# Kernel optimization log

Measured on AMD Instinct MI355X. Metric: run time of the kernel, lower is better.

## Reference

```python
import jax, jax.numpy as jnp
import numpy as np

T, B, D_POSE, H, K_CODES = 30, 1024, 135, 512, 512
EPS = 1e-5


def _bn_relu(x, g, b):
    # BatchNorm1d (training-mode batch stats, biased var) + ReLU; x: (B, C, L)
    m = x.mean(axis=(0, 2), keepdims=True)
    v = x.var(axis=(0, 2), keepdims=True)
    y = g[None, :, None] * (x - m) * jax.lax.rsqrt(v + EPS) + b[None, :, None]
    return jax.nn.relu(y)


def _conv_sk(x, w):
    # Conv1d with stride == kernel_size (non-overlapping): pure reshaped GEMM.
    # x: (B, I, L), w: (O, I, K) torch layout -> (B, O, L//K)
    Bn, I, L = x.shape
    O, _, K = w.shape
    xr = x.reshape(Bn, I, L // K, K)
    return jnp.einsum('bitk,oik->bot', xr, w)


def _convT_sk(x, w):
    # ConvTranspose1d with stride == kernel_size: x (B, I, L), w (I, O, K) torch layout
    Bn, I, L = x.shape
    _, O, K = w.shape
    return jnp.einsum('bil,iok->bolk', x, w).reshape(Bn, O, L * K)


def setup_inputs() -> dict:
    key = jax.random.key(0)
    ks = jax.random.split(key, 12)
    sc = 0.05
    inp = {
        'input_seqs': jax.random.normal(ks[0], (T, B, D_POSE), jnp.float32),
        'W_in': jax.random.normal(ks[1], (D_POSE, H), jnp.float32) * sc,
        'b_in': jnp.zeros((H,), jnp.float32),
        'w_e1': jax.random.normal(ks[2], (H, H, 5), jnp.float32) * sc,
        'g_e1': jnp.ones((H,), jnp.float32), 'b_e1': jnp.zeros((H,), jnp.float32),
        'w_e2': jax.random.normal(ks[3], (H, H, 3), jnp.float32) * sc,
        'g_e2': jnp.ones((H,), jnp.float32), 'b_e2': jnp.zeros((H,), jnp.float32),
        'w_e3': jax.random.normal(ks[4], (H, H, 2), jnp.float32) * sc,
        'g_e3': jnp.ones((H,), jnp.float32), 'b_e3': jnp.zeros((H,), jnp.float32),
        'codebook': jax.random.normal(ks[5], (K_CODES, H), jnp.float32) * sc,
        'W_q': jax.random.normal(ks[6], (H, H), jnp.float32) * sc,
        'b_q': jnp.zeros((H,), jnp.float32),
        'w_d1': jax.random.normal(ks[7], (H, H, 2), jnp.float32) * sc,
        'g_d1': jnp.ones((H,), jnp.float32), 'b_d1': jnp.zeros((H,), jnp.float32),
        'w_d2': jax.random.normal(ks[8], (H, H, 3), jnp.float32) * sc,
        'g_d2': jnp.ones((H,), jnp.float32), 'b_d2': jnp.zeros((H,), jnp.float32),
        'w_d3': jax.random.normal(ks[9], (H, H, 5), jnp.float32) * sc,
        'g_d3': jnp.ones((H,), jnp.float32), 'b_d3': jnp.zeros((H,), jnp.float32),
        'W_out': jax.random.normal(ks[10], (H, D_POSE), jnp.float32) * sc,
        'b_out': jnp.zeros((D_POSE,), jnp.float32),
    }
    return inp


def reference(input_seqs, W_in, b_in, w_e1, g_e1, b_e1, w_e2, g_e2, b_e2,
              w_e3, g_e3, b_e3, codebook, W_q, b_q,
              w_d1, g_d1, b_d1, w_d2, g_d2, b_d2, w_d3, g_d3, b_d3,
              W_out, b_out):
    commitment_cost = 0.25
    # ---- EncoderCNN ----
    h = input_seqs @ W_in + b_in              # (T, B, H)
    h = jnp.transpose(h, (1, 2, 0))           # (B, H, T)
    h = _bn_relu(_conv_sk(h, w_e1), g_e1, b_e1)   # (B, H, 6)
    h = _bn_relu(_conv_sk(h, w_e2), g_e2, b_e2)   # (B, H, 2)
    z = _bn_relu(_conv_sk(h, w_e3), g_e3, b_e3)   # (B, H, 1)

    # ---- VQ (VQ_Payam, straight-through) ----
    Bn, D, L = z.shape
    flat = jnp.transpose(z, (0, 2, 1)).reshape(-1, D)            # (B*L, D)
    dist = (jnp.sum(flat ** 2, axis=1, keepdims=True)
            + jnp.sum(codebook ** 2, axis=1)
            - 2.0 * flat @ codebook.T)                           # (B*L, K)
    idx = jnp.argmin(dist, axis=1)                               # (B*L,)
    quantized = codebook[idx]                                    # (B*L, D)
    e_latent_loss = jnp.mean((jax.lax.stop_gradient(quantized) - flat) ** 2)
    q_latent_loss = jnp.mean((quantized - jax.lax.stop_gradient(flat)) ** 2)
    vq_loss = q_latent_loss + commitment_cost * e_latent_loss
    q_st = flat + jax.lax.stop_gradient(quantized - flat)        # straight-through
    avg_probs = jnp.mean(jax.nn.one_hot(idx, K_CODES, dtype=flat.dtype), axis=0)
    perplexity = jnp.exp(-jnp.sum(avg_probs * jnp.log(avg_probs + 1e-10)))

    # ---- DecoderCNN ----
    d = q_st @ W_q + b_q                      # (B, H)
    d = d[:, :, None]                         # (B, H, 1)
    d = _bn_relu(_convT_sk(d, w_d1), g_d1, b_d1)  # (B, H, 2)
    d = _bn_relu(_convT_sk(d, w_d2), g_d2, b_d2)  # (B, H, 6)
    d = _bn_relu(_convT_sk(d, w_d3), g_d3, b_d3)  # (B, H, 30)
    recon = jnp.transpose(d, (0, 2, 1)) @ W_out + b_out           # (B, T, D_POSE)
    return recon, vq_loss, perplexity
```

## Files before the change

kernel.cpp:

```cpp
#include <hip/hip_runtime.h>
#include <math.h>


typedef __attribute__((ext_vector_type(8))) short bf16x8;
typedef __attribute__((ext_vector_type(4))) float f32x4;

__device__ __forceinline__ unsigned pk_bf16(float a, float b) {
    unsigned ua = __float_as_uint(a), ub = __float_as_uint(b);
    ua += 0x7fffu + ((ua >> 16) & 1u);
    ub += 0x7fffu + ((ub >> 16) & 1u);
    return (ua >> 16) | (ub & 0xffff0000u);
}
__device__ __forceinline__ unsigned short bfh(float x) {
    unsigned u = __float_as_uint(x);
    u += 0x7fffu + ((u >> 16) & 1u);
    return (unsigned short)(u >> 16);
}
__device__ __forceinline__ float bf2f(unsigned short h) {
    return __uint_as_float(((unsigned)h) << 16);
}

template <int NV>
__device__ __forceinline__ void bn_on_raw(uint4* raw, int kbase,
                                          const float* __restrict__ bnS,
                                          const float* __restrict__ bnB) {
#pragma unroll
    for (int i = 0; i < NV; ++i) {
        unsigned* u4 = (unsigned*)&raw[i];
#pragma unroll
        for (int j = 0; j < 4; ++j) {
            const int k = kbase + (i << 3) + (j << 1);
            unsigned u = u4[j];
            float x0 = __uint_as_float(u << 16);
            float x1 = __uint_as_float(u & 0xffff0000u);
            x0 = fmaxf(fmaf(x0, bnS[k],     bnB[k]),     0.f);
            x1 = fmaxf(fmaf(x1, bnS[k + 1], bnB[k + 1]), 0.f);
            u4[j] = pk_bf16(x0, x1);
        }
    }
}

__device__ __forceinline__ void bn4(float4& a, const float* __restrict__ s,
                                    const float* __restrict__ c) {
    float4 sv = *(const float4*)s;
    float4 cv = *(const float4*)c;
    a.x = fmaxf(fmaf(a.x, sv.x, cv.x), 0.f);
    a.y = fmaxf(fmaf(a.y, sv.y, cv.y), 0.f);
    a.z = fmaxf(fmaf(a.z, sv.z, cv.z), 0.f);
    a.w = fmaxf(fmaf(a.w, sv.w, cv.w), 0.f);
}

#define FBK  32
#define FSTR 36

__global__ __launch_bounds__(256)
void k_gemm(const float* __restrict__ Abase,
            const float* __restrict__ Wt,
            float* __restrict__ Cout,
            const float* __restrict__ bnS, const float* __restrict__ bnB,
            unsigned long long* __restrict__ amin,
            const float* __restrict__ codesq,
            int Mslice, int K, int N, int decK)
{
    __shared__ __align__(16) float As[FBK][FSTR];
    __shared__ __align__(16) float Bs[FBK][FSTR];

    const int tid = threadIdx.x;
    const int z  = blockIdx.z;
    const int n0 = blockIdx.x << 5;
    const int m0 = blockIdx.y << 5;
    const int ty = tid >> 4;
    const int tx = tid & 15;

    const int a_slice = z / decK, wk = z - a_slice * decK;
    const float* Ap = Abase + (size_t)a_slice * (size_t)Mslice * (size_t)K;
    const float* Wp = Wt    + (size_t)wk * (size_t)K * (size_t)N;

    const int sr  = tid >> 3;
    const int sc4 = (tid & 7) << 2;

    int mrow = m0 + sr;
    if (mrow > Mslice - 1) mrow = Mslice - 1;
    const float* Arow_p = Ap + (size_t)mrow * K;

    float acc[2][2];
    acc[0][0] = 0.f; acc[0][1] = 0.f; acc[1][0] = 0.f; acc[1][1] = 0.f;

    float4 pa = *(const float4*)(Arow_p + sc4);
    if (bnS != nullptr) bn4(pa, bnS + sc4, bnB + sc4);
    float4 pb = *(const float4*)(Wp + (size_t)sr * N + n0 + sc4);

    for (int k0 = 0; k0 < K; k0 += FBK) {
        __syncthreads();
        As[sc4 + 0][sr] = pa.x;
        As[sc4 + 1][sr] = pa.y;
        As[sc4 + 2][sr] = pa.z;
        As[sc4 + 3][sr] = pa.w;
        *(float4*)&Bs[sr][sc4] = pb;
        const int k0n = k0 + FBK;
        if (k0n < K) {
            pa = *(const float4*)(Arow_p + k0n + sc4);
            if (bnS != nullptr) bn4(pa, bnS + k0n + sc4, bnB + k0n + sc4);
            pb = *(const float4*)(Wp + (size_t)(k0n + sr) * N + n0 + sc4);
        }
        __syncthreads();
#pragma unroll
        for (int kk = 0; kk < FBK; ++kk) {
            float2 av = *(const float2*)&As[kk][ty << 1];
            float2 bv = *(const float2*)&Bs[kk][tx << 1];
            acc[0][0] = fmaf(av.x, bv.x, acc[0][0]);
            acc[0][1] = fmaf(av.x, bv.y, acc[0][1]);
            acc[1][0] = fmaf(av.y, bv.x, acc[1][0]);
            acc[1][1] = fmaf(av.y, bv.y, acc[1][1]);
        }
    }

    if (amin != nullptr) {
        float2 cq = *(const float2*)(codesq + n0 + (tx << 1));
#pragma unroll
        for (int i = 0; i < 2; ++i) {
            const int m = m0 + (ty << 1) + i;
            float d0 = cq.x - 2.f * acc[i][0];
            float d1 = cq.y - 2.f * acc[i][1];
            int bj = (d1 < d0) ? 1 : 0;
            float best = (d1 < d0) ? d1 : d0;
            unsigned u = __float_as_uint(best);
            u = (u & 0x80000000u) ? ~u : (u | 0x80000000u);
            unsigned long long key =
                ((unsigned long long)u << 32) | (unsigned)(n0 + (tx << 1) + bj);
#pragma unroll
            for (int off = 1; off < 16; off <<= 1) {
                unsigned long long o = __shfl_xor(key, off, 64);
                if (o < key) key = o;
            }
            if (tx == 0 && m < Mslice) atomicMin(&amin[m], key);
        }
        return;
    }

#pragma unroll
    for (int i = 0; i < 2; ++i) {
        const int m = m0 + (ty << 1) + i;
        if (m < Mslice) {
            float2 v = make_float2(acc[i][0], acc[i][1]);
            *(float2*)&Cout[((size_t)z * Mslice + m) * N + n0 + (tx << 1)] = v;
        }
    }
}

#define ASTR 72

__global__ __launch_bounds__(256)
void k_mfma_b(const unsigned short* __restrict__ Abase,
              const unsigned short* __restrict__ Bt,
              unsigned short* __restrict__ Cb,
              float* __restrict__ operm,
              const float* __restrict__ bias,
              const float* __restrict__ bnS, const float* __restrict__ bnB,
              float* __restrict__ stats,
              int Mslice, int K, int N, int decK)
{
    __shared__ __align__(16) unsigned short As[128 * ASTR];
    __shared__ __align__(16) unsigned short Bs[128 * ASTR];
    __shared__ float colsum[128], colsq[128];

    const int tid  = threadIdx.x;
    const int lane = tid & 63;
    const int wave = tid >> 6;
    const int wm = (wave >> 1) << 6;
    const int wn = (wave & 1) << 6;
    const int z  = blockIdx.z;
    const int n0 = blockIdx.x << 7;
    const int m0 = blockIdx.y << 7;

    if (stats != nullptr && tid < 128) { colsum[tid] = 0.f; colsq[tid] = 0.f; }

    const int a_slice = z / decK, wk = z - a_slice * decK;
    const unsigned short* Ap = Abase + (size_t)a_slice * (size_t)Mslice * (size_t)K;
    const unsigned short* Bp = Bt + (size_t)wk * (size_t)N * (size_t)K;

    const int sr = tid >> 1;
    const int sk = (tid & 1) << 5;

    const unsigned short* Arow = Ap + (size_t)(m0 + sr) * K + sk;
    const unsigned short* Brow = Bp + (size_t)(n0 + sr) * K + sk;
    const bool bvalid = (n0 + sr) < N;

    f32x4 acc[4][4];
#pragma unroll
    for (int i = 0; i < 4; ++i)
#pragma unroll
        for (int j = 0; j < 4; ++j) acc[i][j] = (f32x4){0.f, 0.f, 0.f, 0.f};

    const int lidx = lane & 15;
    const int lq   = lane >> 4;

    uint4 pa[4], pb[4];
#pragma unroll
    for (int i = 0; i < 4; ++i) pa[i] = *(const uint4*)(Arow + (i << 3));
    if (bnS != nullptr) bn_on_raw<4>(pa, sk, bnS, bnB);
    if (bvalid) {
#pragma unroll
        for (int i = 0; i < 4; ++i) pb[i] = *(const uint4*)(Brow + (i << 3));
    } else {
#pragma unroll
        for (int i = 0; i < 4; ++i) pb[i] = make_uint4(0u, 0u, 0u, 0u);
    }

    for (int k0 = 0; k0 < K; k0 += 64) {
        __syncthreads();
        {
            uint4* dA = (uint4*)&As[sr * ASTR + sk];
            uint4* dB = (uint4*)&Bs[sr * ASTR + sk];
#pragma unroll
            for (int i = 0; i < 4; ++i) { dA[i] = pa[i]; dB[i] = pb[i]; }
        }
        const int k0n = k0 + 64;
        if (k0n < K) {
#pragma unroll
            for (int i = 0; i < 4; ++i) pa[i] = *(const uint4*)(Arow + k0n + (i << 3));
            if (bnS != nullptr) bn_on_raw<4>(pa, k0n + sk, bnS, bnB);
            if (bvalid) {
#pragma unroll
                for (int i = 0; i < 4; ++i) pb[i] = *(const uint4*)(Brow + k0n + (i << 3));
            }
        }
        __syncthreads();
#pragma unroll
        for (int ks = 0; ks < 2; ++ks) {
            const int kb = (ks << 5) + (lq << 3);
            bf16x8 af[4], bfv[4];
#pragma unroll
            for (int t = 0; t < 4; ++t)
                af[t] = *(const bf16x8*)&As[(wm + (t << 4) + lidx) * ASTR + kb];
#pragma unroll
            for (int t = 0; t < 4; ++t)
                bfv[t] = *(const bf16x8*)&Bs[(wn + (t << 4) + lidx) * ASTR + kb];
#pragma unroll
            for (int mt = 0; mt < 4; ++mt)
#pragma unroll
                for (int nt = 0; nt < 4; ++nt)
                    acc[mt][nt] = __builtin_amdgcn_mfma_f32_16x16x32_bf16(
                        af[mt], bfv[nt], acc[mt][nt], 0, 0, 0);
        }
    }

    const int rbase = lq << 2;
#pragma unroll
    for (int nt = 0; nt < 4; ++nt) {
        const int col = n0 + wn + (nt << 4) + lidx;
        const float badd = (bias != nullptr && col < N) ? bias[col] : 0.f;
        float s = 0.f, q = 0.f;
#pragma unroll
        for (int mt = 0; mt < 4; ++mt) {
#pragma unroll
            for (int r = 0; r < 4; ++r) {
                float x = acc[mt][nt][r];
                s += x; q += x * x;
                const int row = m0 + wm + (mt << 4) + rbase + r;
                if (operm != nullptr) {
                    if (col < N) {
                        const int t = row >> 10, b = row & 1023;
                        operm[(size_t)b * 4050 + t * 135 + col] = x + badd;
                    }
                } else {
                    Cb[((size_t)z * Mslice + row) * (size_t)N + col] = bfh(x + badd);
                }
            }
        }
        if (stats != nullptr) {
            s += __shfl_xor(s, 16, 64); s += __shfl_xor(s, 32, 64);
            q += __shfl_xor(q, 16, 64); q += __shfl_xor(q, 32, 64);
            if (lq == 0) {
                atomicAdd(&colsum[wn + (nt << 4) + lidx], s);
                atomicAdd(&colsq [wn + (nt << 4) + lidx], q);
            }
        }
    }
    if (stats != nullptr) {
        __syncthreads();
        if (tid < 128) {
            atomicAdd(&stats[n0 + tid],       colsum[tid]);
            atomicAdd(&stats[512 + n0 + tid], colsq[tid]);
        }
    }
}

#define BSTR 72

__global__ __launch_bounds__(256)
void k_b64(const unsigned short* __restrict__ Abase,
           const unsigned short* __restrict__ Bt,
           unsigned short* __restrict__ Cb,
           const float* __restrict__ bias,
           const float* __restrict__ bnS, const float* __restrict__ bnB,
           float* __restrict__ stats,
           int Mslice, int K, int N, int decK)
{
    __shared__ __align__(16) unsigned short As[64 * BSTR];
    __shared__ __align__(16) unsigned short Bs[64 * BSTR];
    __shared__ float colsum[64], colsq[64];

    const int tid  = threadIdx.x;
    const int lane = tid & 63;
    const int wave = tid >> 6;
    const int wm = (wave >> 1) << 5;
    const int wn = (wave & 1) << 5;
    const int z  = blockIdx.z;
    const int n0 = blockIdx.x << 6;
    const int m0 = blockIdx.y << 6;

    if (stats != nullptr && tid < 64) { colsum[tid] = 0.f; colsq[tid] = 0.f; }

    const int a_slice = z / decK, wk = z - a_slice * decK;
    const unsigned short* Ap = Abase + (size_t)a_slice * (size_t)Mslice * (size_t)K;
    const unsigned short* Bp = Bt + (size_t)wk * (size_t)N * (size_t)K;

    const int sr = tid >> 2;
    const int sk = (tid & 3) << 4;

    const unsigned short* Arow = Ap + (size_t)(m0 + sr) * K + sk;
    const unsigned short* Brow = Bp + (size_t)(n0 + sr) * K + sk;

    f32x4 acc[2][2];
#pragma unroll
    for (int i = 0; i < 2; ++i)
#pragma unroll
        for (int j = 0; j < 2; ++j) acc[i][j] = (f32x4){0.f, 0.f, 0.f, 0.f};

    const int lidx = lane & 15;
    const int lq   = lane >> 4;

    uint4 pa[2], pb[2];
    pa[0] = *(const uint4*)(Arow);
    pa[1] = *(const uint4*)(Arow + 8);
    if (bnS != nullptr) bn_on_raw<2>(pa, sk, bnS, bnB);
    pb[0] = *(const uint4*)(Brow);
    pb[1] = *(const uint4*)(Brow + 8);

    for (int k0 = 0; k0 < K; k0 += 64) {
        __syncthreads();
        {
            uint4* dA = (uint4*)&As[sr * BSTR + sk];
            uint4* dB = (uint4*)&Bs[sr * BSTR + sk];
            dA[0] = pa[0]; dA[1] = pa[1];
            dB[0] = pb[0]; dB[1] = pb[1];
        }
        const int k0n = k0 + 64;
        if (k0n < K) {
            pa[0] = *(const uint4*)(Arow + k0n);
            pa[1] = *(const uint4*)(Arow + k0n + 8);
            if (bnS != nullptr) bn_on_raw<2>(pa, k0n + sk, bnS, bnB);
            pb[0] = *(const uint4*)(Brow + k0n);
            pb[1] = *(const uint4*)(Brow + k0n + 8);
        }
        __syncthreads();
#pragma unroll
        for (int ks = 0; ks < 2; ++ks) {
            const int kb = (ks << 5) + (lq << 3);
            bf16x8 af[2], bfv[2];
#pragma unroll
            for (int t = 0; t < 2; ++t)
                af[t] = *(const bf16x8*)&As[(wm + (t << 4) + lidx) * BSTR + kb];
#pragma unroll
            for (int t = 0; t < 2; ++t)
                bfv[t] = *(const bf16x8*)&Bs[(wn + (t << 4) + lidx) * BSTR + kb];
#pragma unroll
            for (int mt = 0; mt < 2; ++mt)
#pragma unroll
                for (int nt = 0; nt < 2; ++nt)
                    acc[mt][nt] = __builtin_amdgcn_mfma_f32_16x16x32_bf16(
                        af[mt], bfv[nt], acc[mt][nt], 0, 0, 0);
        }
    }

    const int rbase = lq << 2;
#pragma unroll
    for (int nt = 0; nt < 2; ++nt) {
        const int col = n0 + wn + (nt << 4) + lidx;
        const float badd = (bias != nullptr) ? bias[col] : 0.f;
        float s = 0.f, q = 0.f;
#pragma unroll
        for (int mt = 0; mt < 2; ++mt) {
#pragma unroll
            for (int r = 0; r < 4; ++r) {
                float x = acc[mt][nt][r];
                s += x; q += x * x;
                const int row = m0 + wm + (mt << 4) + rbase + r;
                Cb[((size_t)z * Mslice + row) * (size_t)N + col] = bfh(x + badd);
            }
        }
        if (stats != nullptr) {
            s += __shfl_xor(s, 16, 64); s += __shfl_xor(s, 32, 64);
            q += __shfl_xor(q, 16, 64); q += __shfl_xor(q, 32, 64);
            if (lq == 0) {
                atomicAdd(&colsum[wn + (nt << 4) + lidx], s);
                atomicAdd(&colsq [wn + (nt << 4) + lidx], q);
            }
        }
    }
    if (stats != nullptr) {
        __syncthreads();
        if (tid < 64) {
            atomicAdd(&stats[n0 + tid],       colsum[tid]);
            atomicAdd(&stats[512 + n0 + tid], colsq[tid]);
        }
    }
}

#define S64 40

__global__ __launch_bounds__(256)
void k_sp64(const unsigned short* __restrict__ Ahg,
            const unsigned short* __restrict__ Alg,
            const unsigned short* __restrict__ Whi,
            const unsigned short* __restrict__ Wlo,
            float* __restrict__ Cout, float* __restrict__ stats,
            int Mslice, int Kp, int N, int n_terms)
{
    __shared__ __align__(16) unsigned short Ah[64 * S64];
    __shared__ __align__(16) unsigned short Al[64 * S64];
    __shared__ __align__(16) unsigned short Bh[64 * S64];
    __shared__ __align__(16) unsigned short Bl[64 * S64];
    __shared__ float colsum[64], colsq[64];

    const int tid  = threadIdx.x;
    const int lane = tid & 63;
    const int wave = tid >> 6;
    const int wm = (wave >> 1) << 5;
    const int wn = (wave & 1) << 5;
    const int z  = blockIdx.z;
    const int n0 = blockIdx.x << 6;
    const int m0 = blockIdx.y << 6;

    if (stats != nullptr && tid < 64) { colsum[tid] = 0.f; colsq[tid] = 0.f; }

    const int sr = tid >> 2;
    const int sk = (tid & 3) << 3;

    f32x4 acc[2][2];
#pragma unroll
    for (int i = 0; i < 2; ++i)
#pragma unroll
        for (int j = 0; j < 2; ++j) acc[i][j] = (f32x4){0.f, 0.f, 0.f, 0.f};

    const int lidx = lane & 15;
    const int lq   = lane >> 4;
    const int kb   = lq << 3;

    const int cpk = Kp >> 5;
    const int tot = n_terms * cpk;

    uint4 rah, ral, rbh, rblv;
    {
        const size_t ab = ((size_t)(z * n_terms) * Mslice + m0 + sr) * (size_t)Kp + sk;
        rah = *(const uint4*)(Ahg + ab);
        ral = *(const uint4*)(Alg + ab);
        const size_t bb = ((size_t)(n0 + sr)) * (size_t)Kp + sk;
        rbh = *(const uint4*)(Whi + bb);
        rblv = *(const uint4*)(Wlo + bb);
    }
    int lt = 0, lk = 32;
    if (lk >= Kp) { lk = 0; lt = 1; }

    for (int c = 0; c < tot; ++c) {
        __syncthreads();
        *(uint4*)&Ah[sr * S64 + sk] = rah;
        *(uint4*)&Al[sr * S64 + sk] = ral;
        *(uint4*)&Bh[sr * S64 + sk] = rbh;
        *(uint4*)&Bl[sr * S64 + sk] = rblv;
        if (c + 1 < tot) {
            const size_t ab = ((size_t)(z * n_terms + lt) * Mslice + m0 + sr) * (size_t)Kp + lk + sk;
            rah = *(const uint4*)(Ahg + ab);
            ral = *(const uint4*)(Alg + ab);
            const size_t bb = ((size_t)lt * N + n0 + sr) * (size_t)Kp + lk + sk;
            rbh = *(const uint4*)(Whi + bb);
            rblv = *(const uint4*)(Wlo + bb);
            lk += 32; if (lk >= Kp) { lk = 0; ++lt; }
        }
        __syncthreads();
        bf16x8 ah[2], al[2], bh[2], bl[2];
#pragma unroll
        for (int t = 0; t < 2; ++t) {
            const int ra = (wm + (t << 4) + lidx) * S64 + kb;
            ah[t] = *(const bf16x8*)&Ah[ra];
            al[t] = *(const bf16x8*)&Al[ra];
        }
#pragma unroll
        for (int t = 0; t < 2; ++t) {
            const int rb = (wn + (t << 4) + lidx) * S64 + kb;
            bh[t] = *(const bf16x8*)&Bh[rb];
            bl[t] = *(const bf16x8*)&Bl[rb];
        }
#pragma unroll
        for (int mt = 0; mt < 2; ++mt)
#pragma unroll
            for (int nt = 0; nt < 2; ++nt) {
                acc[mt][nt] = __builtin_amdgcn_mfma_f32_16x16x32_bf16(
                    ah[mt], bh[nt], acc[mt][nt], 0, 0, 0);
                acc[mt][nt] = __builtin_amdgcn_mfma_f32_16x16x32_bf16(
                    al[mt], bh[nt], acc[mt][nt], 0, 0, 0);
                acc[mt][nt] = __builtin_amdgcn_mfma_f32_16x16x32_bf16(
                    ah[mt], bl[nt], acc[mt][nt], 0, 0, 0);
            }
    }

    const int rbase = lq << 2;
#pragma unroll
    for (int nt = 0; nt < 2; ++nt) {
        const int col = n0 + wn + (nt << 4) + lidx;
        float s = 0.f, q = 0.f;
#pragma unroll
        for (int mt = 0; mt < 2; ++mt) {
#pragma unroll
            for (int r = 0; r < 4; ++r) {
                float x = acc[mt][nt][r];
                s += x; q += x * x;
                const int row = m0 + wm + (mt << 4) + rbase + r;
                Cout[((size_t)z * Mslice + row) * (size_t)N + col] = x;
            }
        }
        if (stats != nullptr) {
            s += __shfl_xor(s, 16, 64); s += __shfl_xor(s, 32, 64);
            q += __shfl_xor(q, 16, 64); q += __shfl_xor(q, 32, 64);
            if (lq == 0) {
                atomicAdd(&colsum[wn + (nt << 4) + lidx], s);
                atomicAdd(&colsq [wn + (nt << 4) + lidx], q);
            }
        }
    }
    if (stats != nullptr) {
        __syncthreads();
        if (tid < 64) {
            atomicAdd(&stats[n0 + tid],       colsum[tid]);
            atomicAdd(&stats[512 + n0 + tid], colsq[tid]);
        }
    }
}

__global__ void k_prep(float* __restrict__ zbase, unsigned long long* __restrict__ amin,
                       const float* __restrict__ codebook, float* __restrict__ codeT,
                       float* __restrict__ codesq,
                       const float* __restrict__ w_e2, unsigned short* __restrict__ whi_e2,
                       unsigned short* __restrict__ wlo_e2,
                       const float* __restrict__ w_e3, unsigned short* __restrict__ whi_e3,
                       unsigned short* __restrict__ wlo_e3,
                       const float* __restrict__ W_q,  unsigned short* __restrict__ wqb,
                       const float* __restrict__ w_d1, unsigned short* __restrict__ wd1b,
                       const float* __restrict__ w_d2, unsigned short* __restrict__ wd2b,
                       const float* __restrict__ w_d3, unsigned short* __restrict__ wd3b,
                       const float* __restrict__ W_out, unsigned short* __restrict__ woutb,
                       const float* __restrict__ in_seqs,
                       unsigned short* __restrict__ in_h, unsigned short* __restrict__ in_l)
{
    __shared__ float red[4];
    const int bid = blockIdx.x;
    const int tid = threadIdx.x;

    if (bid < 32) {
        int t = bid * 256 + tid;
        if (t < 6720) zbase[t] = 0.f;
        if (t < 1024) amin[t] = ~0ULL;
        return;
    }
    if (bid < 1056) {
        int idx = (bid - 32) * 256 + tid;
        int i = (idx >> 9) & 511, o = idx & 511;
        codeT[idx] = codebook[(o << 9) + i];
        return;
    }
    if (bid < 1568) {
        int c = bid - 1056;
        float s = 0.f;
        for (int i = tid; i < 512; i += 256) { float v = codebook[c * 512 + i]; s += v * v; }
        for (int off = 32; off; off >>= 1) s += __shfl_down(s, off, 64);
        if ((tid & 63) == 0) red[tid >> 6] = s;
        __syncthreads();
        if (tid == 0) codesq[c] = red[0] + red[1] + red[2] + red[3];
        return;
    }
    if (bid < 4640) {
        int idx = (bid - 1568) * 256 + tid;
        int i = idx & 511, o = (idx >> 9) & 511, k = idx >> 18;
        float v = w_e2[(((o << 9) + i) * 3) + k];
        unsigned short h = bfh(v);
        whi_e2[idx] = h; wlo_e2[idx] = bfh(v - bf2f(h));
        return;
    }
    if (bid < 6688) {
        int idx = (bid - 4640) * 256 + tid;
        int i = idx & 511, o = (idx >> 9) & 511, k = idx >> 18;
        float v = w_e3[(((o << 9) + i) * 2) + k];
        unsigned short h = bfh(v);
        whi_e3[idx] = h; wlo_e3[idx] = bfh(v - bf2f(h));
        return;
    }
    if (bid < 7712) {
        int idx = (bid - 6688) * 256 + tid;
        int i = idx & 511, o = (idx >> 9) & 511;
        wqb[idx] = bfh(W_q[((size_t)i << 9) + o]);
        return;
    }
    if (bid < 9760) {
        int idx = (bid - 7712) * 256 + tid;
        int i = idx & 511, o = (idx >> 9) & 511, k = idx >> 18;
        wd1b[idx] = bfh(w_d1[(((size_t)i << 9) + o) * 2 + k]);
        return;
    }
    if (bid < 12832) {
        int idx = (bid - 9760) * 256 + tid;
        int i = idx & 511, o = (idx >> 9) & 511, k = idx >> 18;
        wd2b[idx] = bfh(w_d2[(((size_t)i << 9) + o) * 3 + k]);
        return;
    }
    if (bid < 17952) {
        int idx = (bid - 12832) * 256 + tid;
        int i = idx & 511, o = (idx >> 9) & 511, k = idx >> 18;
        wd3b[idx] = bfh(w_d3[(((size_t)i << 9) + o) * 5 + k]);
        return;
    }
    if (bid < 18222) {
        int idx = (bid - 17952) * 256 + tid;
        if (idx >= 69120) return;
        int i = idx % 512, o = idx / 512;
        woutb[idx] = bfh(W_out[((size_t)i * 135) + o]);
        return;
    }
    {
        int idx = (bid - 18222) * 256 + tid;
        if (idx >= 4915200) return;
        int i = idx % 160, r = idx / 160;
        float v = (i < 135) ? in_seqs[(size_t)r * 135 + i] : 0.f;
        unsigned short h = bfh(v);
        in_h[idx] = h; in_l[idx] = bfh(v - bf2f(h));
    }
}

__global__ void k_repack(const float* __restrict__ w, float* __restrict__ wt,
                         int Kc, int total)
{
    int idx = blockIdx.x * 256 + threadIdx.x;
    if (idx >= total) return;
    int k = idx >> 18;
    int rem = idx & 262143;
    int i = rem >> 9, o = rem & 511;
    wt[idx] = w[(((o << 9) + i) * Kc + k)];
}

__global__ void k_repack_sp_weff(const float* __restrict__ weff,
                                 unsigned short* __restrict__ whi,
                                 unsigned short* __restrict__ wlo,
                                 int total)
{
    int idx = blockIdx.x * 256 + threadIdx.x;
    if (idx >= total) return;
    int i = idx % 160;
    int o = (idx / 160) & 511;
    int t = idx / 81920;
    float v = (i < 135) ? weff[((size_t)t * 135 + i) * 512 + o] : 0.f;
    unsigned short h = bfh(v);
    whi[idx] = h;
    wlo[idx] = bfh(v - bf2f(h));
}

__global__ void k_bnsplit(const float* __restrict__ x,
                          const float* __restrict__ sc, const float* __restrict__ sh,
                          unsigned short* __restrict__ hq, unsigned short* __restrict__ lq_,
                          int total4)
{
    int idx = blockIdx.x * 256 + threadIdx.x;
    if (idx >= total4) return;
    const int base = idx << 2;
    float4 f = *(const float4*)(x + base);
    const int k = base & 511;
    float4 s = *(const float4*)(sc + k);
    float4 c = *(const float4*)(sh + k);
    float y0 = fmaxf(fmaf(f.x, s.x, c.x), 0.f);
    float y1 = fmaxf(fmaf(f.y, s.y, c.y), 0.f);
    float y2 = fmaxf(fmaf(f.z, s.z, c.z), 0.f);
    float y3 = fmaxf(fmaf(f.w, s.w, c.w), 0.f);
    unsigned short h0 = bfh(y0), h1 = bfh(y1), h2 = bfh(y2), h3 = bfh(y3);
    unsigned short l0 = bfh(y0 - bf2f(h0)), l1 = bfh(y1 - bf2f(h1));
    unsigned short l2 = bfh(y2 - bf2f(h2)), l3 = bfh(y3 - bf2f(h3));
    *(uint2*)&hq[base]  = make_uint2((unsigned)h0 | ((unsigned)h1 << 16),
                                     (unsigned)h2 | ((unsigned)h3 << 16));
    *(uint2*)&lq_[base] = make_uint2((unsigned)l0 | ((unsigned)l1 << 16),
                                     (unsigned)l2 | ((unsigned)l3 << 16));
}

__global__ void k_bnapply(const unsigned short* __restrict__ x,
                          const float* __restrict__ sc, const float* __restrict__ sh,
                          unsigned short* __restrict__ y, int total8)
{
    int idx = blockIdx.x * 256 + threadIdx.x;
    if (idx >= total8) return;
    const int base = idx << 3;
    uint4 raw = *(const uint4*)(x + base);
    const int k = base & 511;
    float4 s0 = *(const float4*)(sc + k);
    float4 c0 = *(const float4*)(sh + k);
    float4 s1 = *(const float4*)(sc + k + 4);
    float4 c1 = *(const float4*)(sh + k + 4);
    unsigned* u = (unsigned*)&raw;
    float x0 = __uint_as_float(u[0] << 16),        x1 = __uint_as_float(u[0] & 0xffff0000u);
    float x2 = __uint_as_float(u[1] << 16),        x3 = __uint_as_float(u[1] & 0xffff0000u);
    float x4 = __uint_as_float(u[2] << 16),        x5 = __uint_as_float(u[2] & 0xffff0000u);
    float x6 = __uint_as_float(u[3] << 16),        x7 = __uint_as_float(u[3] & 0xffff0000u);
    x0 = fmaxf(fmaf(x0, s0.x, c0.x), 0.f); x1 = fmaxf(fmaf(x1, s0.y, c0.y), 0.f);
    x2 = fmaxf(fmaf(x2, s0.z, c0.z), 0.f); x3 = fmaxf(fmaf(x3, s0.w, c0.w), 0.f);
    x4 = fmaxf(fmaf(x4, s1.x, c1.x), 0.f); x5 = fmaxf(fmaf(x5, s1.y, c1.y), 0.f);
    x6 = fmaxf(fmaf(x6, s1.z, c1.z), 0.f); x7 = fmaxf(fmaf(x7, s1.w, c1.w), 0.f);
    *(uint4*)&y[base] = make_uint4(pk_bf16(x0, x1), pk_bf16(x2, x3),
                                   pk_bf16(x4, x5), pk_bf16(x6, x7));
}

__global__ void k_bn_fin(const float* __restrict__ stats,
                         const float* __restrict__ g, const float* __restrict__ b,
                         float* __restrict__ sc, float* __restrict__ sh, float inv_n)
{
    int c = blockIdx.x * blockDim.x + threadIdx.x;
    if (c >= 512) return;
    float m = stats[c] * inv_n;
    float v = stats[512 + c] * inv_n - m * m;
    float a = (float)((double)g[c] / sqrt((double)v + 1e-5));
    sc[c] = a;
    sh[c] = b[c] - m * a;
}

__global__ void k_vq_gather(const unsigned long long* __restrict__ amin,
                            const float* __restrict__ codebook,
                            const float* __restrict__ e3pre,
                            const float* __restrict__ sc, const float* __restrict__ sh,
                            unsigned short* __restrict__ quant_bf,
                            float* __restrict__ loss,
                            unsigned int* __restrict__ hist)
{
    int b = blockIdx.x; int t = threadIdx.x;
    unsigned int idx = (unsigned int)(amin[b] & 0xFFFFFFFFull) & 511u;
    float part = 0.f;
    for (int i = t; i < 512; i += 256) {
        float q = codebook[(size_t)idx * 512 + i];
        quant_bf[(size_t)b * 512 + i] = bfh(q);
        float x = e3pre[(size_t)b * 512 + i];
        float f = fmaxf(fmaf(x, sc[i], sh[i]), 0.f);
        float d = q - f;
        part += d * d;
    }
    for (int off = 32; off; off >>= 1) part += __shfl_down(part, off, 64);
    __shared__ float red[4];
    if ((t & 63) == 0) red[t >> 6] = part;
    __syncthreads();
    if (t == 0) {
        atomicAdd(loss, red[0] + red[1] + red[2] + red[3]);
        atomicAdd(&hist[idx], 1u);
    }
}

__global__ void k_scalars(const unsigned int* __restrict__ hist,
                          const float* __restrict__ loss, float* __restrict__ out)
{
    int t = threadIdx.x;
    float p = (float)hist[t] * (1.0f / 1024.0f);
    float e = p * logf(p + 1e-10f);
    for (int off = 32; off; off >>= 1) e += __shfl_down(e, off, 64);
    __shared__ float red[8];
    if ((t & 63) == 0) red[t >> 6] = e;
    __syncthreads();
    if (t == 0) {
        float s = 0.f;
        for (int i = 0; i < 8; ++i) s += red[i];
        out[4147200] = 1.25f * loss[0] * (1.0f / 524288.0f);
        out[4147201] = expf(-s);
    }
}

extern "C" void kernel_launch(void* const* d_in, const int* in_sizes, int n_in,
                              void* d_out, int out_size, void* d_ws, size_t ws_size,
                              hipStream_t stream)
{
    const float* in_seqs = (const float*)d_in[0];
    const float* W_in  = (const float*)d_in[1];
    const float* w_e1  = (const float*)d_in[3];
    const float* g_e1  = (const float*)d_in[4];
    const float* be1   = (const float*)d_in[5];
    const float* w_e2  = (const float*)d_in[6];
    const float* g_e2  = (const float*)d_in[7];
    const float* be2   = (const float*)d_in[8];
    const float* w_e3  = (const float*)d_in[9];
    const float* g_e3  = (const float*)d_in[10];
    const float* be3   = (const float*)d_in[11];
    const float* codebook = (const float*)d_in[12];
    const float* W_q   = (const float*)d_in[13];
    const float* b_q   = (const float*)d_in[14];
    const float* w_d1  = (const float*)d_in[15];
    const float* g_d1  = (const float*)d_in[16];
    const float* bd1   = (const float*)d_in[17];
    const float* w_d2  = (const float*)d_in[18];
    const float* g_d2  = (const float*)d_in[19];
    const float* bd2   = (const float*)d_in[20];
    const float* w_d3  = (const float*)d_in[21];
    const float* g_d3  = (const float*)d_in[22];
    const float* bd3   = (const float*)d_in[23];
    const float* W_out = (const float*)d_in[24];
    const float* b_out = (const float*)d_in[25];
    float* out = (float*)d_out;

    float* W = (float*)d_ws;
    unsigned long long* amin = (unsigned long long*)W;
    float* stats  = W + 2048;
    float* lossp  = W + 8192;
    unsigned int* hist = (unsigned int*)(W + 8256);
    float* scsh   = W + 8768;
    float* codesq = W + 14912;
    float* wt_e1  = W + 15424;
    float* weff   = W + 1326144;
    float* codeT  = W + 1671744;
    unsigned short* esw = (unsigned short*)(W + 1933888);
    unsigned short* whi_e1 = esw;
    unsigned short* wlo_e1 = esw + 409600;
    unsigned short* whi_e2 = esw + 819200;
    unsigned short* wlo_e2 = esw + 1605632;
    unsigned short* whi_e3 = esw + 2392064;
    unsigned short* wlo_e3 = esw + 2916352;
    unsigned short* in_h  = (unsigned short*)(W + 3654208);
    unsigned short* in_l  = in_h + 4915200;
    unsigned short* d3pre = (unsigned short*)(W + 3654208);
    float* e1f = W + 11518528;
    unsigned short* e1h = (unsigned short*)(W + 14664256);
    unsigned short* e1l = e1h + 3145728;
    float* e2f = W + 17809984;
    unsigned short* e2h = (unsigned short*)(W + 18858560);
    unsigned short* e2l = e2h + 1048576;
    unsigned short* d2pre = (unsigned short*)(W + 17809984);
    unsigned short* d2bf  = d2pre + 3145728;
    float* e3f = W + 20955712;
    unsigned short* quant_bf = (unsigned short*)(W + 21480000);
    unsigned short* d0bf     = (unsigned short*)(W + 21742144);
    unsigned short* d1pre    = (unsigned short*)(W + 22004288);

    unsigned short* db    = (unsigned short*)wt_e1;
    unsigned short* wqb   = db;
    unsigned short* wd1b  = db + 262144;
    unsigned short* wd2b  = db + 786432;
    unsigned short* wd3b  = db + 1572864;
    unsigned short* woutb = db + 2883584;

    float* st_e1 = stats + 0 * 1024; float* sc_e1 = scsh + 0 * 1024; float* sh_e1 = sc_e1 + 512;
    float* st_e2 = stats + 1 * 1024; float* sc_e2 = scsh + 1 * 1024; float* sh_e2 = sc_e2 + 512;
    float* st_e3 = stats + 2 * 1024; float* sc_e3 = scsh + 2 * 1024; float* sh_e3 = sc_e3 + 512;
    float* st_d1 = stats + 3 * 1024; float* sc_d1 = scsh + 3 * 1024; float* sh_d1 = sc_d1 + 512;
    float* st_d2 = stats + 4 * 1024; float* sc_d2 = scsh + 4 * 1024; float* sh_d2 = sc_d2 + 512;
    float* st_d3 = stats + 5 * 1024; float* sc_d3 = scsh + 5 * 1024; float* sh_d3 = sc_d3 + 512;

    dim3 blk(256);

    k_repack<<<dim3(5 * 1024), blk, 0, stream>>>(w_e1, wt_e1, 5, 5 * 262144);
    k_gemm<<<dim3(16, 5, 5), blk, 0, stream>>>(W_in, wt_e1, weff,
        nullptr, nullptr, nullptr, nullptr, 135, 512, 512, 5);
    k_repack_sp_weff<<<dim3(1600), blk, 0, stream>>>(weff, whi_e1, wlo_e1, 409600);

    k_prep<<<dim3(37422), blk, 0, stream>>>(stats, amin,
        codebook, codeT, codesq,
        w_e2, whi_e2, wlo_e2, w_e3, whi_e3, wlo_e3,
        W_q, wqb, w_d1, wd1b, w_d2, wd2b, w_d3, wd3b, W_out, woutb,
        in_seqs, in_h, in_l);

    k_sp64<<<dim3(8, 16, 6), blk, 0, stream>>>(in_h, in_l, whi_e1, wlo_e1,
        e1f, st_e1, 1024, 160, 512, 5);
    k_bn_fin<<<dim3(2), blk, 0, stream>>>(st_e1, g_e1, be1, sc_e1, sh_e1, 1.f / 6144.f);
    k_bnsplit<<<dim3(3072), blk, 0, stream>>>(e1f, sc_e1, sh_e1, e1h, e1l, 786432);

    k_sp64<<<dim3(8, 16, 2), blk, 0, stream>>>(e1h, e1l, whi_e2, wlo_e2,
        e2f, st_e2, 1024, 512, 512, 3);
    k_bn_fin<<<dim3(2), blk, 0, stream>>>(st_e2, g_e2, be2, sc_e2, sh_e2, 1.f / 2048.f);
    k_bnsplit<<<dim3(1024), blk, 0, stream>>>(e2f, sc_e2, sh_e2, e2h, e2l, 262144);

    k_sp64<<<dim3(8, 16, 1), blk, 0, stream>>>(e2h, e2l, whi_e3, wlo_e3,
        e3f, st_e3, 1024, 512, 512, 2);
    k_bn_fin<<<dim3(2), blk, 0, stream>>>(st_e3, g_e3, be3, sc_e3, sh_e3, 1.f / 1024.f);

    k_gemm<<<dim3(16, 32, 1), blk, 0, stream>>>(e3f, codeT, nullptr,
        sc_e3, sh_e3, amin, codesq, 1024, 512, 512, 1);
    k_vq_gather<<<dim3(1024), blk, 0, stream>>>(amin, codebook, e3f, sc_e3, sh_e3,
                                                quant_bf, lossp, hist);

    k_b64<<<dim3(8, 16, 1), blk, 0, stream>>>(quant_bf, wqb, d0bf,
        b_q, nullptr, nullptr, nullptr, 1024, 512, 512, 1);

    k_b64<<<dim3(8, 16, 2), blk, 0, stream>>>(d0bf, wd1b, d1pre,
        nullptr, nullptr, nullptr, st_d1, 1024, 512, 512, 2);
    k_bn_fin<<<dim3(2), blk, 0, stream>>>(st_d1, g_d1, bd1, sc_d1, sh_d1, 1.f / 2048.f);

    k_b64<<<dim3(8, 16, 6), blk, 0, stream>>>(d1pre, wd2b, d2pre,
        nullptr, sc_d1, sh_d1, st_d2, 1024, 512, 512, 3);
    k_bn_fin<<<dim3(2), blk, 0, stream>>>(st_d2, g_d2, bd2, sc_d2, sh_d2, 1.f / 6144.f);

    k_bnapply<<<dim3(1536), blk, 0, stream>>>(d2pre, sc_d2, sh_d2, d2bf, 393216);

    k_mfma_b<<<dim3(4, 8, 30), blk, 0, stream>>>(d2bf, wd3b, d3pre, nullptr,
        nullptr, nullptr, nullptr, st_d3, 1024, 512, 512, 5);
    k_bn_fin<<<dim3(2), blk, 0, stream>>>(st_d3, g_d3, bd3, sc_d3, sh_d3, 1.f / 30720.f);

    k_mfma_b<<<dim3(2, 240, 1), blk, 0, stream>>>(d3pre, woutb, nullptr, out,
        b_out, sc_d3, sh_d3, nullptr, 30720, 512, 135, 1);

    k_scalars<<<dim3(1), dim3(512), 0, stream>>>(hist, lossp, out);
}
```

Baseline: 457.3 us.

## Load GEMM tiles via direct global-to-LDS with XOR swizzle; hoist BN to separate passes

The MFMA GEMM kernels now stage A and B tiles with global_load_lds (direct global-to-shared loads) into unpadded, XOR-swizzled LDS layouts instead of a register prefetch plus store. The swizzle keeps fragment reads free of bank conflicts. Because BN+ReLU can no longer be applied in registers during loading, it moves into separate k_bnapply passes that write bf16 copies of d1 and d3. This adds extra kernel launches and a full read/write of the large d3 tensor, and drops the register double-buffering overlap in exchange for a simpler load path.

```diff
diff --git a/kernel.cpp b/kernel.cpp
--- a/kernel.cpp
+++ b/kernel.cpp
@@ -20,24 +20,10 @@
     return __uint_as_float(((unsigned)h) << 16);
 }
 
-template <int NV>
-__device__ __forceinline__ void bn_on_raw(uint4* raw, int kbase,
-                                          const float* __restrict__ bnS,
-                                          const float* __restrict__ bnB) {
-#pragma unroll
-    for (int i = 0; i < NV; ++i) {
-        unsigned* u4 = (unsigned*)&raw[i];
-#pragma unroll
-        for (int j = 0; j < 4; ++j) {
-            const int k = kbase + (i << 3) + (j << 1);
-            unsigned u = u4[j];
-            float x0 = __uint_as_float(u << 16);
-            float x1 = __uint_as_float(u & 0xffff0000u);
-            x0 = fmaxf(fmaf(x0, bnS[k],     bnB[k]),     0.f);
-            x1 = fmaxf(fmaf(x1, bnS[k + 1], bnB[k + 1]), 0.f);
-            u4[j] = pk_bf16(x0, x1);
-        }
-    }
+__device__ __forceinline__ void gload16(const unsigned short* g, unsigned short* l) {
+    __builtin_amdgcn_global_load_lds(
+        (const __attribute__((address_space(1))) unsigned int*)g,
+        (__attribute__((address_space(3))) unsigned int*)l, 16, 0, 0);
 }
 
 __device__ __forceinline__ void bn4(float4& a, const float* __restrict__ s,
@@ -148,20 +134,17 @@
     }
 }
 
-#define ASTR 72
-
 __global__ __launch_bounds__(256)
-void k_mfma_b(const unsigned short* __restrict__ Abase,
+void k_mfma_g(const unsigned short* __restrict__ Abase,
               const unsigned short* __restrict__ Bt,
               unsigned short* __restrict__ Cb,
               float* __restrict__ operm,
               const float* __restrict__ bias,
-              const float* __restrict__ bnS, const float* __restrict__ bnB,
               float* __restrict__ stats,
               int Mslice, int K, int N, int decK)
 {
-    __shared__ __align__(16) unsigned short As[128 * ASTR];
-    __shared__ __align__(16) unsigned short Bs[128 * ASTR];
+    __shared__ __align__(16) unsigned short As[128 * 64];
+    __shared__ __align__(16) unsigned short Bs[128 * 64];
     __shared__ float colsum[128], colsq[128];
 
     const int tid  = threadIdx.x;
@@ -179,12 +162,19 @@
     const unsigned short* Ap = Abase + (size_t)a_slice * (size_t)Mslice * (size_t)K;
     const unsigned short* Bp = Bt + (size_t)wk * (size_t)N * (size_t)K;
 
-    const int sr = tid >> 1;
-    const int sk = (tid & 1) << 5;
-
-    const unsigned short* Arow = Ap + (size_t)(m0 + sr) * K + sk;
-    const unsigned short* Brow = Bp + (size_t)(n0 + sr) * K + sk;
-    const bool bvalid = (n0 + sr) < N;
+    const int srow  = tid >> 3;
+    const int selem = ((tid & 7) ^ (srow & 7)) << 3;
+    const unsigned short* Asrc = Ap + (size_t)(m0 + srow) * K + selem;
+    unsigned short* Adst = As + tid * 8;
+    unsigned short* Bdst = Bs + tid * 8;
+
+    size_t boff[4];
+#pragma unroll
+    for (int c = 0; c < 4; ++c) {
+        int brow = n0 + srow + (c << 5);
+        if (brow > N - 1) brow = N - 1;
+        boff[c] = (size_t)brow * K + selem;
+    }
 
     f32x4 acc[4][4];
 #pragma unroll
@@ -195,47 +185,25 @@
     const int lidx = lane & 15;
     const int lq   = lane >> 4;
 
-    uint4 pa[4], pb[4];
-#pragma unroll
-    for (int i = 0; i < 4; ++i) pa[i] = *(const uint4*)(Arow + (i << 3));
-    if (bnS != nullptr) bn_on_raw<4>(pa, sk, bnS, bnB);
-    if (bvalid) {
-#pragma unroll
-        for (int i = 0; i < 4; ++i) pb[i] = *(const uint4*)(Brow + (i << 3));
-    } else {
-#pragma unroll
-        for (int i = 0; i < 4; ++i) pb[i] = make_uint4(0u, 0u, 0u, 0u);
-    }
-
     for (int k0 = 0; k0 < K; k0 += 64) {
         __syncthreads();
-        {
-            uint4* dA = (uint4*)&As[sr * ASTR + sk];
-            uint4* dB = (uint4*)&Bs[sr * ASTR + sk];
-#pragma unroll
-            for (int i = 0; i < 4; ++i) { dA[i] = pa[i]; dB[i] = pb[i]; }
-        }
-        const int k0n = k0 + 64;
-        if (k0n < K) {
-#pragma unroll
-            for (int i = 0; i < 4; ++i) pa[i] = *(const uint4*)(Arow + k0n + (i << 3));
-            if (bnS != nullptr) bn_on_raw<4>(pa, k0n + sk, bnS, bnB);
-            if (bvalid) {
-#pragma unroll
-                for (int i = 0; i < 4; ++i) pb[i] = *(const uint4*)(Brow + k0n + (i << 3));
-            }
+#pragma unroll
+        for (int c = 0; c < 4; ++c) {
+            gload16(Asrc + (size_t)(c << 5) * K + k0, Adst + (c << 11));
+            gload16(Bp + boff[c] + k0, Bdst + (c << 11));
         }
         __syncthreads();
 #pragma unroll
         for (int ks = 0; ks < 2; ++ks) {
-            const int kb = (ks << 5) + (lq << 3);
+            const int ub = (ks << 2) + lq;
+            const int uo = (ub ^ (lidx & 7)) << 3;
             bf16x8 af[4], bfv[4];
 #pragma unroll
             for (int t = 0; t < 4; ++t)
-                af[t] = *(const bf16x8*)&As[(wm + (t << 4) + lidx) * ASTR + kb];
+                af[t] = *(const bf16x8*)&As[((wm + (t << 4) + lidx) << 6) + uo];
 #pragma unroll
             for (int t = 0; t < 4; ++t)
-                bfv[t] = *(const bf16x8*)&Bs[(wn + (t << 4) + lidx) * ASTR + kb];
+                bfv[t] = *(const bf16x8*)&Bs[((wn + (t << 4) + lidx) << 6) + uo];
 #pragma unroll
             for (int mt = 0; mt < 4; ++mt)
 #pragma unroll
@@ -286,19 +254,16 @@
     }
 }
 
-#define BSTR 72
-
 __global__ __launch_bounds__(256)
-void k_b64(const unsigned short* __restrict__ Abase,
-           const unsigned short* __restrict__ Bt,
-           unsigned short* __restrict__ Cb,
-           const float* __restrict__ bias,
-           const float* __restrict__ bnS, const float* __restrict__ bnB,
-           float* __restrict__ stats,
-           int Mslice, int K, int N, int decK)
-{
-    __shared__ __align__(16) unsigned short As[64 * BSTR];
-    __shared__ __align__(16) unsigned short Bs[64 * BSTR];
+void k_b64g(const unsigned short* __restrict__ Abase,
+            const unsigned short* __restrict__ Bt,
+            unsigned short* __restrict__ Cb,
+            const float* __restrict__ bias,
+            float* __restrict__ stats,
+            int Mslice, int K, int N, int decK)
+{
+    __shared__ __align__(16) unsigned short As[64 * 64];
+    __shared__ __align__(16) unsigned short Bs[64 * 64];
     __shared__ float colsum[64], colsq[64];
 
     const int tid  = threadIdx.x;
@@ -316,11 +281,12 @@
     const unsigned short* Ap = Abase + (size_t)a_slice * (size_t)Mslice * (size_t)K;
     const unsigned short* Bp = Bt + (size_t)wk * (size_t)N * (size_t)K;
 
-    const int sr = tid >> 2;
-    const int sk = (tid & 3) << 4;
-
-    const unsigned short* Arow = Ap + (size_t)(m0 + sr) * K + sk;
-    const unsigned short* Brow = Bp + (size_t)(n0 + sr) * K + sk;
+    const int srow  = tid >> 3;
+    const int selem = ((tid & 7) ^ (srow & 7)) << 3;
+    const unsigned short* Asrc = Ap + (size_t)(m0 + srow) * K + selem;
+    const unsigned short* Bsrc = Bp + (size_t)(n0 + srow) * K + selem;
+    unsigned short* Adst = As + tid * 8;
+    unsigned short* Bdst = Bs + tid * 8;
 
     f32x4 acc[2][2];
 #pragma unroll
@@ -331,40 +297,25 @@
     const int lidx = lane & 15;
     const int lq   = lane >> 4;
 
-    uint4 pa[2], pb[2];
-    pa[0] = *(const uint4*)(Arow);
-    pa[1] = *(const uint4*)(Arow + 8);
-    if (bnS != nullptr) bn_on_raw<2>(pa, sk, bnS, bnB);
-    pb[0] = *(const uint4*)(Brow);
-    pb[1] = *(const uint4*)(Brow + 8);
-
     for (int k0 = 0; k0 < K; k0 += 64) {
         __syncthreads();
-        {
-            uint4* dA = (uint4*)&As[sr * BSTR + sk];
-            uint4* dB = (uint4*)&Bs[sr * BSTR + sk];
-            dA[0] = pa[0]; dA[1] = pa[1];
-            dB[0] = pb[0]; dB[1] = pb[1];
-        }
-        const int k0n = k0 + 64;
-        if (k0n < K) {
-            pa[0] = *(const uint4*)(Arow + k0n);
-            pa[1] = *(const uint4*)(Arow + k0n + 8);
-            if (bnS != nullptr) bn_on_raw<2>(pa, k0n + sk, bnS, bnB);
-            pb[0] = *(const uint4*)(Brow + k0n);
-            pb[1] = *(const uint4*)(Brow + k0n + 8);
+#pragma unroll
+        for (int c = 0; c < 2; ++c) {
+            gload16(Asrc + (size_t)(c << 5) * K + k0, Adst + (c << 11));
+            gload16(Bsrc + (size_t)(c << 5) * K + k0, Bdst + (c << 11));
         }
         __syncthreads();
 #pragma unroll
         for (int ks = 0; ks < 2; ++ks) {
-            const int kb = (ks << 5) + (lq << 3);
+            const int ub = (ks << 2) + lq;
+            const int uo = (ub ^ (lidx & 7)) << 3;
             bf16x8 af[2], bfv[2];
 #pragma unroll
             for (int t = 0; t < 2; ++t)
-                af[t] = *(const bf16x8*)&As[(wm + (t << 4) + lidx) * BSTR + kb];
+                af[t] = *(const bf16x8*)&As[((wm + (t << 4) + lidx) << 6) + uo];
 #pragma unroll
             for (int t = 0; t < 2; ++t)
-                bfv[t] = *(const bf16x8*)&Bs[(wn + (t << 4) + lidx) * BSTR + kb];
+                bfv[t] = *(const bf16x8*)&Bs[((wn + (t << 4) + lidx) << 6) + uo];
 #pragma unroll
             for (int mt = 0; mt < 2; ++mt)
 #pragma unroll
@@ -408,20 +359,18 @@
     }
 }
 
-#define S64 40
-
 __global__ __launch_bounds__(256)
-void k_sp64(const unsigned short* __restrict__ Ahg,
-            const unsigned short* __restrict__ Alg,
-            const unsigned short* __restrict__ Whi,
-            const unsigned short* __restrict__ Wlo,
-            float* __restrict__ Cout, float* __restrict__ stats,
-            int Mslice, int Kp, int N, int n_terms)
-{
-    __shared__ __align__(16) unsigned short Ah[64 * S64];
-    __shared__ __align__(16) unsigned short Al[64 * S64];
-    __shared__ __align__(16) unsigned short Bh[64 * S64];
-    __shared__ __align__(16) unsigned short Bl[64 * S64];
+void k_sp64g(const unsigned short* __restrict__ Ahg,
+             const unsigned short* __restrict__ Alg,
+             const unsigned short* __restrict__ Whi,
+             const unsigned short* __restrict__ Wlo,
+             float* __restrict__ Cout, float* __restrict__ stats,
+             int Mslice, int Kp, int N, int n_terms)
+{
+    __shared__ __align__(16) unsigned short Ah[64 * 32];
+    __shared__ __align__(16) unsigned short Al[64 * 32];
+    __shared__ __align__(16) unsigned short Bh[64 * 32];
+    __shared__ __align__(16) unsigned short Bl[64 * 32];
     __shared__ float colsum[64], colsq[64];
 
     const int tid  = threadIdx.x;
@@ -435,8 +384,12 @@
 
     if (stats != nullptr && tid < 64) { colsum[tid] = 0.f; colsq[tid] = 0.f; }
 
-    const int sr = tid >> 2;
-    const int sk = (tid & 3) << 3;
+    const int srow  = tid >> 2;
+    const int selem = ((tid & 3) ^ (srow & 3)) << 3;
+    unsigned short* Ahd = Ah + tid * 8;
+    unsigned short* Ald = Al + tid * 8;
+    unsigned short* Bhd = Bh + tid * 8;
+    unsigned short* Bld = Bl + tid * 8;
 
     f32x4 acc[2][2];
 #pragma unroll
@@ -446,49 +399,35 @@
 
     const int lidx = lane & 15;
     const int lq   = lane >> 4;
-    const int kb   = lq << 3;
+    const int uo   = (lq ^ (lidx & 3)) << 3;
 
     const int cpk = Kp >> 5;
     const int tot = n_terms * cpk;
 
-    uint4 rah, ral, rbh, rblv;
-    {
-        const size_t ab = ((size_t)(z * n_terms) * Mslice + m0 + sr) * (size_t)Kp + sk;
-        rah = *(const uint4*)(Ahg + ab);
-        ral = *(const uint4*)(Alg + ab);
-        const size_t bb = ((size_t)(n0 + sr)) * (size_t)Kp + sk;
-        rbh = *(const uint4*)(Whi + bb);
-        rblv = *(const uint4*)(Wlo + bb);
-    }
-    int lt = 0, lk = 32;
-    if (lk >= Kp) { lk = 0; lt = 1; }
-
+    int lt = 0, lk = 0;
     for (int c = 0; c < tot; ++c) {
         __syncthreads();
-        *(uint4*)&Ah[sr * S64 + sk] = rah;
-        *(uint4*)&Al[sr * S64 + sk] = ral;
-        *(uint4*)&Bh[sr * S64 + sk] = rbh;
-        *(uint4*)&Bl[sr * S64 + sk] = rblv;
-        if (c + 1 < tot) {
-            const size_t ab = ((size_t)(z * n_terms + lt) * Mslice + m0 + sr) * (size_t)Kp + lk + sk;
-            rah = *(const uint4*)(Ahg + ab);
-            ral = *(const uint4*)(Alg + ab);
-            const size_t bb = ((size_t)lt * N + n0 + sr) * (size_t)Kp + lk + sk;
-            rbh = *(const uint4*)(Whi + bb);
-            rblv = *(const uint4*)(Wlo + bb);
-            lk += 32; if (lk >= Kp) { lk = 0; ++lt; }
-        }
+        {
+            const size_t ab = ((size_t)(z * n_terms + lt) * Mslice + m0 + srow)
+                              * (size_t)Kp + lk + selem;
+            const size_t bb = ((size_t)lt * N + n0 + srow) * (size_t)Kp + lk + selem;
+            gload16(Ahg + ab, Ahd);
+            gload16(Alg + ab, Ald);
+            gload16(Whi + bb, Bhd);
+            gload16(Wlo + bb, Bld);
+        }
+        lk += 32; if (lk >= Kp) { lk = 0; ++lt; }
         __syncthreads();
         bf16x8 ah[2], al[2], bh[2], bl[2];
 #pragma unroll
         for (int t = 0; t < 2; ++t) {
-            const int ra = (wm + (t << 4) + lidx) * S64 + kb;
+            const int ra = ((wm + (t << 4) + lidx) << 5) + uo;
             ah[t] = *(const bf16x8*)&Ah[ra];
             al[t] = *(const bf16x8*)&Al[ra];
         }
 #pragma unroll
         for (int t = 0; t < 2; ++t) {
-            const int rb = (wn + (t << 4) + lidx) * S64 + kb;
+            const int rb = ((wn + (t << 4) + lidx) << 5) + uo;
             bh[t] = *(const bf16x8*)&Bh[rb];
             bl[t] = *(const bf16x8*)&Bl[rb];
         }
@@ -837,6 +776,8 @@
     unsigned short* quant_bf = (unsigned short*)(W + 21480000);
     unsigned short* d0bf     = (unsigned short*)(W + 21742144);
     unsigned short* d1pre    = (unsigned short*)(W + 22004288);
+    unsigned short* d1bf     = (unsigned short*)(W + 22528640);
+    unsigned short* d3bf     = (unsigned short*)(W + 23052928);
 
     unsigned short* db    = (unsigned short*)wt_e1;
     unsigned short* wqb   = db;
@@ -865,17 +806,17 @@
         W_q, wqb, w_d1, wd1b, w_d2, wd2b, w_d3, wd3b, W_out, woutb,
         in_seqs, in_h, in_l);
 
-    k_sp64<<<dim3(8, 16, 6), blk, 0, stream>>>(in_h, in_l, whi_e1, wlo_e1,
+    k_sp64g<<<dim3(8, 16, 6), blk, 0, stream>>>(in_h, in_l, whi_e1, wlo_e1,
         e1f, st_e1, 1024, 160, 512, 5);
     k_bn_fin<<<dim3(2), blk, 0, stream>>>(st_e1, g_e1, be1, sc_e1, sh_e1, 1.f / 6144.f);
     k_bnsplit<<<dim3(3072), blk, 0, stream>>>(e1f, sc_e1, sh_e1, e1h, e1l, 786432);
 
-    k_sp64<<<dim3(8, 16, 2), blk, 0, stream>>>(e1h, e1l, whi_e2, wlo_e2,
+    k_sp64g<<<dim3(8, 16, 2), blk, 0, stream>>>(e1h, e1l, whi_e2, wlo_e2,
         e2f, st_e2, 1024, 512, 512, 3);
     k_bn_fin<<<dim3(2), blk, 0, stream>>>(st_e2, g_e2, be2, sc_e2, sh_e2, 1.f / 2048.f);
     k_bnsplit<<<dim3(1024), blk, 0, stream>>>(e2f, sc_e2, sh_e2, e2h, e2l, 262144);
 
-    k_sp64<<<dim3(8, 16, 1), blk, 0, stream>>>(e2h, e2l, whi_e3, wlo_e3,
+    k_sp64g<<<dim3(8, 16, 1), blk, 0, stream>>>(e2h, e2l, whi_e3, wlo_e3,
         e3f, st_e3, 1024, 512, 512, 2);
     k_bn_fin<<<dim3(2), blk, 0, stream>>>(st_e3, g_e3, be3, sc_e3, sh_e3, 1.f / 1024.f);
 
@@ -884,25 +825,26 @@
     k_vq_gather<<<dim3(1024), blk, 0, stream>>>(amin, codebook, e3f, sc_e3, sh_e3,
                                                 quant_bf, lossp, hist);
 
-    k_b64<<<dim3(8, 16, 1), blk, 0, stream>>>(quant_bf, wqb, d0bf,
-        b_q, nullptr, nullptr, nullptr, 1024, 512, 512, 1);
-
-    k_b64<<<dim3(8, 16, 2), blk, 0, stream>>>(d0bf, wd1b, d1pre,
-        nullptr, nullptr, nullptr, st_d1, 1024, 512, 512, 2);
+    k_b64g<<<dim3(8, 16, 1), blk, 0, stream>>>(quant_bf, wqb, d0bf,
+        b_q, nullptr, 1024, 512, 512, 1);
+
+    k_b64g<<<dim3(8, 16, 2), blk, 0, stream>>>(d0bf, wd1b, d1pre,
+        nullptr, st_d1, 1024, 512, 512, 2);
     k_bn_fin<<<dim3(2), blk, 0, stream>>>(st_d1, g_d1, bd1, sc_d1, sh_d1, 1.f / 2048.f);
-
-    k_b64<<<dim3(8, 16, 6), blk, 0, stream>>>(d1pre, wd2b, d2pre,
-        nullptr, sc_d1, sh_d1, st_d2, 1024, 512, 512, 3);
+    k_bnapply<<<dim3(512), blk, 0, stream>>>(d1pre, sc_d1, sh_d1, d1bf, 131072);
+
+    k_b64g<<<dim3(8, 16, 6), blk, 0, stream>>>(d1bf, wd2b, d2pre,
+        nullptr, st_d2, 1024, 512, 512, 3);
     k_bn_fin<<<dim3(2), blk, 0, stream>>>(st_d2, g_d2, bd2, sc_d2, sh_d2, 1.f / 6144.f);
-
     k_bnapply<<<dim3(1536), blk, 0, stream>>>(d2pre, sc_d2, sh_d2, d2bf, 393216);
 
-    k_mfma_b<<<dim3(4, 8, 30), blk, 0, stream>>>(d2bf, wd3b, d3pre, nullptr,
-        nullptr, nullptr, nullptr, st_d3, 1024, 512, 512, 5);
+    k_mfma_g<<<dim3(4, 8, 30), blk, 0, stream>>>(d2bf, wd3b, d3pre,
+        nullptr, nullptr, st_d3, 1024, 512, 512, 5);
     k_bn_fin<<<dim3(2), blk, 0, stream>>>(st_d3, g_d3, bd3, sc_d3, sh_d3, 1.f / 30720.f);
-
-    k_mfma_b<<<dim3(2, 240, 1), blk, 0, stream>>>(d3pre, woutb, nullptr, out,
-        b_out, sc_d3, sh_d3, nullptr, 30720, 512, 135, 1);
+    k_bnapply<<<dim3(7680), blk, 0, stream>>>(d3pre, sc_d3, sh_d3, d3bf, 1966080);
+
+    k_mfma_g<<<dim3(2, 240, 1), blk, 0, stream>>>(d3bf, woutb, nullptr,
+        out, b_out, nullptr, 30720, 512, 135, 1);
 
     k_scalars<<<dim3(1), dim3(512), 0, stream>>>(hist, lossp, out);
 }
```

After: 442.6 us. 1.03x faster.
